# Performance work log

Hardware: AMD Instinct MI355X
Metric: run time of the kernel (lower is better)

The kernel has to match this reference:

```python
import jax, jax.numpy as jnp
import numpy as np

N = 10000          # num nodes
E = 640000         # num edges (avg degree 64)
IN_CH = 128
OUT_CH = 128


def setup_inputs() -> dict:
    key = jax.random.key(0)
    k_x, k_ei, k_ea, k_w1, k_b1, k_w2, k_b2 = jax.random.split(key, 7)
    x = jax.random.normal(k_x, (N, IN_CH), dtype=jnp.float32)
    edge_index = jax.random.randint(k_ei, (2, E), 0, N, dtype=jnp.int64)
    edge_attr = jax.random.uniform(k_ea, (E,), dtype=jnp.float32)
    # MLP params: Linear(2*in, out) -> ReLU -> Linear(out, out), stored as [in, out]
    s1 = 1.0 / np.sqrt(2 * IN_CH)
    s2 = 1.0 / np.sqrt(OUT_CH)
    W1 = jax.random.uniform(k_w1, (2 * IN_CH, OUT_CH), jnp.float32, -s1, s1)
    b1 = jax.random.uniform(k_b1, (OUT_CH,), jnp.float32, -s1, s1)
    W2 = jax.random.uniform(k_w2, (OUT_CH, OUT_CH), jnp.float32, -s2, s2)
    b2 = jax.random.uniform(k_b2, (OUT_CH,), jnp.float32, -s2, s2)
    return {"x": x, "edge_index": edge_index, "edge_attr": edge_attr,
            "W1": W1, "b1": b1, "W2": W2, "b2": b2}


def reference(x, edge_index, edge_attr, W1, b1, W2, b2):
    row, col = edge_index[0], edge_index[1]
    # message: scale sender feature by edge_attr, concat with receiver feature, 2-layer MLP
    x_i = x[row] * edge_attr[:, None]          # [E, in]
    x_j = x[col]                               # [E, in]
    combined = jnp.concatenate([x_i, x_j], axis=1)  # [E, 2*in]
    h = jax.nn.relu(combined @ W1 + b1)        # [E, out]
    messages = h @ W2 + b2                     # [E, out]
    # sum aggregation: scatter-add messages into receiving nodes (col)
    out = jnp.zeros((x.shape[0], messages.shape[1]), dtype=messages.dtype)
    out = out.at[col].add(messages)
    return out
```

## Files before the change

kernel.cpp:

```cpp
#include <hip/hip_runtime.h>

#define C 128
#define NPB 16
#define CAP 128
#define OVF_MAX 65536
#define EPT1 16
#define GSH 4
#define G (1 << GSH)
#define CAPB 2048
#define MAXBIN 1024
#define BCS 16


__device__ __forceinline__ unsigned bf16_bits(float x) {
    unsigned u = __float_as_uint(x);
    u += 0x7FFFu + ((u >> 16) & 1u);
    return u >> 16;
}

__global__ void fused_pre_kernel(const float* __restrict__ x, const float* __restrict__ W1,
                                 unsigned short* __restrict__ P16, float* __restrict__ Q,
                                 const int* __restrict__ ei, const float* __restrict__ attr,
                                 uint2* __restrict__ bins, int* __restrict__ bin_cursor,
                                 int* __restrict__ ovf_cnt, int2* __restrict__ ovf,
                                 int N, int E, int PBLK, int NBIN) {
    if ((int)blockIdx.x < PBLK) {
        __shared__ int hist[MAXBIN];
        __shared__ int boff[MAXBIN];
        for (int i = threadIdx.x; i < NBIN; i += 256) { hist[i] = 0; boff[i] = 0; }
        __syncthreads();
        const int base = ((int)blockIdx.x * 256 + (int)threadIdx.x) * EPT1;
        const int rem = (base < E) ? min(EPT1, E - base) : 0;
        const bool vec = (rem == EPT1) && ((E & 3) == 0);
        if (vec) {
#pragma unroll
            for (int j0 = 0; j0 < EPT1; j0 += 4) {
                const int4 c = *(const int4*)(ei + (size_t)E + base + j0);
                atomicAdd(&hist[c.x >> GSH], 1);
                atomicAdd(&hist[c.y >> GSH], 1);
                atomicAdd(&hist[c.z >> GSH], 1);
                atomicAdd(&hist[c.w >> GSH], 1);
            }
        } else {
            for (int j = 0; j < rem; ++j)
                atomicAdd(&hist[ei[(size_t)E + base + j] >> GSH], 1);
        }
        __syncthreads();
        for (int i = threadIdx.x; i < NBIN; i += 256) {
            const int c = hist[i];
            int b = 0;
            if (c) {
                const int cp = (c + 7) & ~7;
                b = atomicAdd(&bin_cursor[i * BCS], cp);
                for (int k = c; k < cp; ++k)
                    if (b + k < CAPB)
                        bins[(size_t)i * CAPB + b + k] = make_uint2(0u, 0xFFFFFFFFu);
            }
            hist[i] = b;
        }
        __syncthreads();
        if (vec) {
#pragma unroll
            for (int j0 = 0; j0 < EPT1; j0 += 4) {
                const int4 r = *(const int4*)(ei + base + j0);
                const int4 c = *(const int4*)(ei + (size_t)E + base + j0);
                const float4 a = *(const float4*)(attr + base + j0);
                const int rr[4] = {r.x, r.y, r.z, r.w};
                const int cc[4] = {c.x, c.y, c.z, c.w};
                const float aa[4] = {a.x, a.y, a.z, a.w};
#pragma unroll
                for (int j = 0; j < 4; ++j) {
                    const int bin = cc[j] >> GSH;
                    const int idx = hist[bin] + atomicAdd(&boff[bin], 1);
                    const unsigned pk = (bf16_bits(aa[j]) << 16) | (unsigned)rr[j];
                    if (idx < CAPB) {
                        bins[(size_t)bin * CAPB + idx] = make_uint2(pk, (unsigned)cc[j]);
                    } else {
                        const int o = atomicAdd(ovf_cnt, 1);
                        if (o < OVF_MAX) ovf[o] = make_int2(cc[j], (int)pk);
                    }
                }
            }
        } else {
            for (int j = 0; j < rem; ++j) {
                const int row = ei[base + j], colv = ei[(size_t)E + base + j];
                const int bin = colv >> GSH;
                const int idx = hist[bin] + atomicAdd(&boff[bin], 1);
                const unsigned pk = (bf16_bits(attr[base + j]) << 16) | (unsigned)row;
                if (idx < CAPB) {
                    bins[(size_t)bin * CAPB + idx] = make_uint2(pk, (unsigned)colv);
                } else {
                    const int o = atomicAdd(ovf_cnt, 1);
                    if (o < OVF_MAX) ovf[o] = make_int2(colv, (int)pk);
                }
            }
        }
    } else {
        __shared__ float xs[NPB][C];
        const int pb = (int)blockIdx.x - PBLK;
        const int n0 = pb * NPB;
        for (int i = threadIdx.x; i < NPB * C; i += 256) {
            const int gi = n0 * C + i;
            xs[0][i] = (gi < N * C) ? x[gi] : 0.f;
        }
        __syncthreads();
        const int col4 = threadIdx.x & 63;
        const int jg   = threadIdx.x >> 6;
        const bool isQ = col4 >= 32;
        const int c0   = (isQ ? (col4 - 32) : col4) << 2;
        const float* __restrict__ Wb = W1 + (isQ ? (C * C) : 0) + c0;
        float acc[4][4] = {};
        for (int k = 0; k < C; k += 4) {
            const float4 w0 = *(const float4*)(Wb + (size_t)(k + 0) * C);
            const float4 w1 = *(const float4*)(Wb + (size_t)(k + 1) * C);
            const float4 w2 = *(const float4*)(Wb + (size_t)(k + 2) * C);
            const float4 w3 = *(const float4*)(Wb + (size_t)(k + 3) * C);
#pragma unroll
            for (int j = 0; j < 4; ++j) {
                const float4 xv = *(const float4*)(&xs[jg * 4 + j][k]);
                acc[j][0] = fmaf(xv.x, w0.x, fmaf(xv.y, w1.x, fmaf(xv.z, w2.x, fmaf(xv.w, w3.x, acc[j][0]))));
                acc[j][1] = fmaf(xv.x, w0.y, fmaf(xv.y, w1.y, fmaf(xv.z, w2.y, fmaf(xv.w, w3.y, acc[j][1]))));
                acc[j][2] = fmaf(xv.x, w0.z, fmaf(xv.y, w1.z, fmaf(xv.z, w2.z, fmaf(xv.w, w3.z, acc[j][2]))));
                acc[j][3] = fmaf(xv.x, w0.w, fmaf(xv.y, w1.w, fmaf(xv.z, w2.w, fmaf(xv.w, w3.w, acc[j][3]))));
            }
        }
#pragma unroll
        for (int j = 0; j < 4; ++j) {
            const int n = n0 + jg * 4 + j;
            if (n < N) {
                if (isQ) {
                    *(float4*)(Q + (size_t)n * C + c0) =
                        make_float4(acc[j][0], acc[j][1], acc[j][2], acc[j][3]);
                } else {
                    ushort4 s;
                    s.x = (unsigned short)bf16_bits(acc[j][0]);
                    s.y = (unsigned short)bf16_bits(acc[j][1]);
                    s.z = (unsigned short)bf16_bits(acc[j][2]);
                    s.w = (unsigned short)bf16_bits(acc[j][3]);
                    *(ushort4*)(P16 + (size_t)n * C + c0) = s;
                }
            }
        }
    }
}

__global__ void bin_agg_out_kernel(const uint2* __restrict__ bins, const int* __restrict__ bin_cursor,
                                   const unsigned short* __restrict__ P16, const float* __restrict__ Q,
                                   const float* __restrict__ b1, const float* __restrict__ W2,
                                   const float* __restrict__ b2,
                                   int* __restrict__ ovf_cnt, int2* __restrict__ ovf,
                                   float* __restrict__ out, int N) {
    __shared__ unsigned smem[G][C];
    __shared__ int off[G];
    float* __restrict__ smemf = (float*)&smem[0][0];
    const int t = threadIdx.x;
    const int b = blockIdx.x;
    const int n0 = b << GSH;
    if (t < G) off[t] = 0;
    __syncthreads();
    const int cnt = min(bin_cursor[b * BCS], CAPB);
    const uint2* __restrict__ src = bins + (size_t)b * CAPB;
#define PLACE(e)                                                                         \
    {                                                                                    \
        const unsigned noff = (e).y - (unsigned)n0;                                      \
        if (noff < (unsigned)G) {                            \
            const int pos = atomicAdd(&off[noff], 1);                                    \
            if (pos < CAP) {                                                             \
                smem[noff][pos] = (e).x;                                                 \
            } else {                                                                     \
                const int o = atomicAdd(ovf_cnt, 1);                                     \
                if (o < OVF_MAX) ovf[o] = make_int2((int)(e).y, (int)(e).x);             \
            }                                                                            \
        }                                                                                \
    }
    {
        int i = t;
        for (; i + 256 < cnt; i += 512) {
            const uint2 ea = src[i];
            const uint2 eb = src[i + 256];
            PLACE(ea);
            PLACE(eb);
        }
        if (i < cnt) {
            const uint2 ea = src[i];
            PLACE(ea);
        }
    }
#undef PLACE
    __syncthreads();
    const int g = t >> 4;
    const int ch8 = t & 15;
    const int n = n0 + g;
#define LD(ew) (*(const uint4*)(P16 + (((size_t)((ew) & 0xFFFFu)) << 7) + (ch8 << 3)))
#define PROC(ew, p, qb0, qb1)                                                            \
    {                                                                                    \
        const float a_ = __uint_as_float((ew) & 0xFFFF0000u);                            \
        acc0.x += fmaxf(fmaf(a_, __uint_as_float((p).x << 16),         qb0.x), 0.f);     \
        acc0.y += fmaxf(fmaf(a_, __uint_as_float((p).x & 0xFFFF0000u), qb0.y), 0.f);     \
        acc0.z += fmaxf(fmaf(a_, __uint_as_float((p).y << 16),         qb0.z), 0.f);     \
        acc0.w += fmaxf(fmaf(a_, __uint_as_float((p).y & 0xFFFF0000u), qb0.w), 0.f);     \
        acc1.x += fmaxf(fmaf(a_, __uint_as_float((p).z << 16),         qb1.x), 0.f);     \
        acc1.y += fmaxf(fmaf(a_, __uint_as_float((p).z & 0xFFFF0000u), qb1.y), 0.f);     \
        acc1.z += fmaxf(fmaf(a_, __uint_as_float((p).w << 16),         qb1.z), 0.f);     \
        acc1.w += fmaxf(fmaf(a_, __uint_as_float((p).w & 0xFFFF0000u), qb1.w), 0.f);     \
    }
    float4 acc0 = make_float4(0.f, 0.f, 0.f, 0.f);
    float4 acc1 = acc0;
    int degp = 0, mcnt = 0;
    if (n < N) {
        degp = min(off[g], CAP);
        const float4 qlo = *(const float4*)(Q + (size_t)n * C + (ch8 << 3));
        const float4 qhi = *(const float4*)(Q + (size_t)n * C + (ch8 << 3) + 4);
        const float4 blo = *(const float4*)(b1 + (ch8 << 3));
        const float4 bhi = *(const float4*)(b1 + (ch8 << 3) + 4);
        const float4 qb0 = make_float4(qlo.x + blo.x, qlo.y + blo.y, qlo.z + blo.z, qlo.w + blo.w);
        const float4 qb1 = make_float4(qhi.x + bhi.x, qhi.y + bhi.y, qhi.z + bhi.z, qhi.w + bhi.w);
        int i = 0;
        if (degp >= 4) {
            uint4 e4 = *(const uint4*)(&smem[g][0]);
            uint4 p0 = LD(e4.x), p1 = LD(e4.y), p2 = LD(e4.z), p3 = LD(e4.w);
            for (i = 4; i + 4 <= degp; i += 4) {
                const uint4 e4n = *(const uint4*)(&smem[g][i]);
                const uint4 q0 = LD(e4n.x), q1 = LD(e4n.y),
                            q2 = LD(e4n.z), q3 = LD(e4n.w);
                PROC(e4.x, p0, qb0, qb1);
                PROC(e4.y, p1, qb0, qb1);
                PROC(e4.z, p2, qb0, qb1);
                PROC(e4.w, p3, qb0, qb1);
                e4 = e4n; p0 = q0; p1 = q1; p2 = q2; p3 = q3;
            }
            PROC(e4.x, p0, qb0, qb1);
            PROC(e4.y, p1, qb0, qb1);
            PROC(e4.z, p2, qb0, qb1);
            PROC(e4.w, p3, qb0, qb1);
        }
        for (; i < degp; ++i) {
            const unsigned ew = smem[g][i];
            const uint4 p = LD(ew);
            PROC(ew, p, qb0, qb1);
        }
        const int oc = min(*ovf_cnt, OVF_MAX);
        for (int o = 0; o < oc; ++o) {
            const int2 v = ovf[o];
            if (v.x == n) {
                ++mcnt;
                const unsigned ew = (unsigned)v.y;
                const uint4 p = LD(ew);
                PROC(ew, p, qb0, qb1);
            }
        }
        *(float4*)(smemf + g * C + (ch8 << 3))     = acc0;
        *(float4*)(smemf + g * C + (ch8 << 3) + 4) = acc1;
        if (ch8 == 0) off[g] = degp + mcnt;
    }
#undef PROC
#undef LD
    __syncthreads();
    const int col = t & (C - 1);
    const int half = t >> 7;
    float acc[8] = {};
    for (int k = 0; k < C; k += 4) {
        const float w0 = W2[(k + 0) * C + col];
        const float w1 = W2[(k + 1) * C + col];
        const float w2v = W2[(k + 2) * C + col];
        const float w3 = W2[(k + 3) * C + col];
#pragma unroll
        for (int j = 0; j < 8; ++j) {
            const float4 h4 = *(const float4*)(smemf + (half * 8 + j) * C + k);
            acc[j] = fmaf(h4.x, w0, fmaf(h4.y, w1, fmaf(h4.z, w2v, fmaf(h4.w, w3, acc[j]))));
        }
    }
    const float bv = b2[col];
#pragma unroll
    for (int j = 0; j < 8; ++j) {
        const int n2 = n0 + half * 8 + j;
        if (n2 < N) out[(size_t)n2 * C + col] = fmaf((float)off[half * 8 + j], bv, acc[j]);
    }
}

extern "C" void kernel_launch(void* const* d_in, const int* in_sizes, int n_in,
                              void* d_out, int out_size, void* d_ws, size_t ws_size,
                              hipStream_t stream) {
    const float* x    = (const float*)d_in[0];
    const int*   ei   = (const int*)d_in[1];
    const float* attr = (const float*)d_in[2];
    const float* W1   = (const float*)d_in[3];
    const float* b1   = (const float*)d_in[4];
    const float* W2   = (const float*)d_in[5];
    const float* b2   = (const float*)d_in[6];
    float* out = (float*)d_out;

    const int N = in_sizes[0] / C;
    const int E = in_sizes[2];
    const int NBIN = (N + G - 1) >> GSH;

    char* ws = (char*)d_ws;
    unsigned short* P16 = (unsigned short*)ws;  ws += (size_t)N * C * sizeof(unsigned short);
    ws = (char*)(((uintptr_t)ws + 15) & ~(uintptr_t)15);
    float*    Q       = (float*)ws;     ws += (size_t)N * C * sizeof(float);
    uint2*    bins    = (uint2*)ws;     ws += (size_t)NBIN * CAPB * sizeof(uint2);
    int2*     ovf     = (int2*)ws;      ws += (size_t)OVF_MAX * sizeof(int2);
    int*      bin_cursor = (int*)ws;    ws += (size_t)NBIN * BCS * sizeof(int);
    int*      ovf_cnt = (int*)ws;

    hipMemsetAsync(bin_cursor, 0, ((size_t)NBIN * BCS + 1) * sizeof(int), stream);

    const int PBLK = (E + 256 * EPT1 - 1) / (256 * EPT1);
    const int PB = (N + NPB - 1) / NPB;
    fused_pre_kernel<<<PBLK + PB, 256, 0, stream>>>(x, W1, P16, Q, ei, attr,
                                                    bins, bin_cursor, ovf_cnt, ovf,
                                                    N, E, PBLK, NBIN);
    bin_agg_out_kernel<<<NBIN, 256, 0, stream>>>(bins, bin_cursor, P16, Q, b1, W2, b2,
                                                 ovf_cnt, ovf, out, N);
}
```

Before: 132.6 us.

## Stage binned edges in shared memory for coalesced global scatter

The binning phase now computes a block-local exclusive prefix scan over per-bin counts and writes each edge into a shared-memory staging buffer ordered by bin. A second pass then has consecutive threads copy consecutive staged entries to their global bin slots, so global writes become mostly contiguous instead of scattered per edge. This adds a 256-step-log scan with several barriers and 32KB of extra shared memory per block, which may reduce occupancy.

```diff
diff --git a/kernel.cpp b/kernel.cpp
--- a/kernel.cpp
+++ b/kernel.cpp
@@ -26,10 +26,15 @@
                                  int N, int E, int PBLK, int NBIN) {
     if ((int)blockIdx.x < PBLK) {
         __shared__ int hist[MAXBIN];
+        __shared__ int lstart[MAXBIN];
         __shared__ int boff[MAXBIN];
-        for (int i = threadIdx.x; i < NBIN; i += 256) { hist[i] = 0; boff[i] = 0; }
-        __syncthreads();
-        const int base = ((int)blockIdx.x * 256 + (int)threadIdx.x) * EPT1;
+        __shared__ int scan[256];
+        __shared__ int ltot;
+        __shared__ uint2 staged[256 * EPT1];
+        const int t = threadIdx.x;
+        for (int i = t; i < NBIN; i += 256) { hist[i] = 0; boff[i] = 0; }
+        __syncthreads();
+        const int base = ((int)blockIdx.x * 256 + t) * EPT1;
         const int rem = (base < E) ? min(EPT1, E - base) : 0;
         const bool vec = (rem == EPT1) && ((E & 3) == 0);
         if (vec) {
@@ -46,7 +51,29 @@
                 atomicAdd(&hist[ei[(size_t)E + base + j] >> GSH], 1);
         }
         __syncthreads();
-        for (int i = threadIdx.x; i < NBIN; i += 256) {
+        int sum = 0;
+#pragma unroll
+        for (int k = 0; k < MAXBIN / 256; ++k) {
+            const int i = (t << 2) + k;
+            if (i < NBIN) sum += hist[i];
+        }
+        scan[t] = sum;
+        __syncthreads();
+        for (int o = 1; o < 256; o <<= 1) {
+            const int v = (t >= o) ? scan[t - o] : 0;
+            __syncthreads();
+            scan[t] += v;
+            __syncthreads();
+        }
+        int run = scan[t] - sum;
+#pragma unroll
+        for (int k = 0; k < MAXBIN / 256; ++k) {
+            const int i = (t << 2) + k;
+            if (i < NBIN) { lstart[i] = run; run += hist[i]; }
+        }
+        if (t == 255) ltot = scan[255];
+        __syncthreads();
+        for (int i = t; i < NBIN; i += 256) {
             const int c = hist[i];
             int b = 0;
             if (c) {
@@ -58,7 +85,6 @@
             }
             hist[i] = b;
         }
-        __syncthreads();
         if (vec) {
 #pragma unroll
             for (int j0 = 0; j0 < EPT1; j0 += 4) {
@@ -71,28 +97,31 @@
 #pragma unroll
                 for (int j = 0; j < 4; ++j) {
                     const int bin = cc[j] >> GSH;
-                    const int idx = hist[bin] + atomicAdd(&boff[bin], 1);
+                    const int lidx = atomicAdd(&boff[bin], 1);
                     const unsigned pk = (bf16_bits(aa[j]) << 16) | (unsigned)rr[j];
-                    if (idx < CAPB) {
-                        bins[(size_t)bin * CAPB + idx] = make_uint2(pk, (unsigned)cc[j]);
-                    } else {
-                        const int o = atomicAdd(ovf_cnt, 1);
-                        if (o < OVF_MAX) ovf[o] = make_int2(cc[j], (int)pk);
-                    }
+                    staged[lstart[bin] + lidx] = make_uint2(pk, (unsigned)cc[j]);
                 }
             }
         } else {
             for (int j = 0; j < rem; ++j) {
                 const int row = ei[base + j], colv = ei[(size_t)E + base + j];
                 const int bin = colv >> GSH;
-                const int idx = hist[bin] + atomicAdd(&boff[bin], 1);
+                const int lidx = atomicAdd(&boff[bin], 1);
                 const unsigned pk = (bf16_bits(attr[base + j]) << 16) | (unsigned)row;
-                if (idx < CAPB) {
-                    bins[(size_t)bin * CAPB + idx] = make_uint2(pk, (unsigned)colv);
-                } else {
-                    const int o = atomicAdd(ovf_cnt, 1);
-                    if (o < OVF_MAX) ovf[o] = make_int2(colv, (int)pk);
-                }
+                staged[lstart[bin] + lidx] = make_uint2(pk, (unsigned)colv);
+            }
+        }
+        __syncthreads();
+        const int lt = ltot;
+        for (int pos = t; pos < lt; pos += 256) {
+            const uint2 e = staged[pos];
+            const int bin = (int)(e.y >> GSH);
+            const int dst = hist[bin] + (pos - lstart[bin]);
+            if (dst < CAPB) {
+                bins[(size_t)bin * CAPB + dst] = e;
+            } else {
+                const int o = atomicAdd(ovf_cnt, 1);
+                if (o < OVF_MAX) ovf[o] = make_int2((int)e.y, (int)e.x);
             }
         }
     } else {
```

Measured after the change: 142.3 us. 7.3% more time.
